# Performance work log

Measured on AMD Instinct MI355X. Metric: run time of the kernel, lower is better.

Reference implementation:

```python
import jax, jax.numpy as jnp
import numpy as np

WS = 4           # window_size
NUM_HEADS = 4
LN_EPS = 1e-5


def setup_inputs() -> dict:
    key = jax.random.key(0)
    ks = jax.random.split(key, 8)
    d = 256
    s = 0.02
    return {
        "feature": jax.random.normal(ks[0], (8, d, 127, 127), dtype=jnp.float32),
        "ln_w": jnp.ones((d,), jnp.float32),
        "ln_b": jnp.zeros((d,), jnp.float32),
        "in_w": jax.random.normal(ks[1], (3 * d, d), jnp.float32) * s,
        "in_b": jnp.zeros((3 * d,), jnp.float32),
        "out_w": jax.random.normal(ks[2], (d, d), jnp.float32) * s,
        "out_b": jnp.zeros((d,), jnp.float32),
        "proj_w": jax.random.normal(ks[3], (d, d), jnp.float32) * s,
        "proj_b": jnp.zeros((d,), jnp.float32),
    }


def reference(feature, ln_w, ln_b, in_w, in_b, out_w, out_b, proj_w, proj_b):
    B, C, H, W = feature.shape
    ws = WS
    pad_h = (-H) % ws
    pad_w = (-W) % ws
    x = jnp.pad(feature, ((0, 0), (0, 0), (0, pad_h), (0, pad_w)))
    Hp, Wp = H + pad_h, W + pad_w
    nh, nw = Hp // ws, Wp // ws
    # NCHW -> NHWC -> windows [B*nh*nw, ws*ws, C]
    x = x.transpose(0, 2, 3, 1)
    win = (x.reshape(B, nh, ws, nw, ws, C)
            .transpose(0, 1, 3, 2, 4, 5)
            .reshape(-1, ws * ws, C))
    # LayerNorm (ddof=0, matches torch)
    mu = win.mean(-1, keepdims=True)
    var = win.var(-1, keepdims=True)
    xn = (win - mu) / jnp.sqrt(var + LN_EPS) * ln_w + ln_b
    # fused QKV projection, then split heads
    qkv = xn @ in_w.T + in_b
    q, k, v = jnp.split(qkv, 3, axis=-1)
    hd = C // NUM_HEADS
    def heads(t):
        return t.reshape(t.shape[0], t.shape[1], NUM_HEADS, hd).transpose(0, 2, 1, 3)
    q, k, v = heads(q), heads(k), heads(v)
    scores = jnp.einsum('bhqd,bhkd->bhqk', q, k) / np.float32(np.sqrt(hd))
    a = jax.nn.softmax(scores, axis=-1)
    o = jnp.einsum('bhqk,bhkd->bhqd', a, v)
    o = o.transpose(0, 2, 1, 3).reshape(-1, ws * ws, C)
    o = o @ out_w.T + out_b
    # residual + Linear + exact GELU
    y = win + jax.nn.gelu(o @ proj_w.T + proj_b, approximate=False)
    # windows -> NHWC, crop padding, -> NCHW
    y = (y.reshape(B, nh, nw, ws, ws, C)
          .transpose(0, 1, 3, 2, 4, 5)
          .reshape(B, Hp, Wp, C))
    return y[:, :H, :W, :].transpose(0, 3, 1, 2)
```

## Files before the change

kernel.cpp:

```cpp
#include <hip/hip_runtime.h>

typedef _Float16 f16;
typedef __attribute__((ext_vector_type(4))) _Float16 half4;
typedef __attribute__((ext_vector_type(8))) _Float16 half8;
typedef __attribute__((ext_vector_type(4))) float f32x4;
typedef unsigned short u16;

#define MFMA32(a,b,c) __builtin_amdgcn_mfma_f32_16x16x32_f16(a,b,c,0,0,0)
#define MFMA16(a,b,c) __builtin_amdgcn_mfma_f32_16x16x16f16(a,b,c,0,0,0)

#define W_IN0   0
#define W_OUT0  196608
#define W_PROJ0 262144
#define X0      327680
#define QK0     33882112ull
#define VT0     100990976ull

__device__ __forceinline__ float gelu_f(float x) {
    float z = x * 0.70710678118f;
    float az = fabsf(z);
    float t = 1.f / (1.f + 0.3275911f * az);
    float e = __expf(-z * z);
    float poly = ((((1.061405429f * t - 1.453152027f) * t + 1.421413741f) * t
                   - 0.284496736f) * t + 0.254829592f) * t;
    float er = 1.f - poly * e;
    er = copysignf(er, z);
    return 0.5f * x * (1.f + er);
}

__global__ void k0_cast(const float* __restrict__ iw, const float* __restrict__ ow,
                        const float* __restrict__ pw, f16* __restrict__ W) {
    int i = blockIdx.x * 256 + threadIdx.x;
    if (i < 196608) W[W_IN0 + i] = (f16)iw[i];
    if (i < 16384) {
        const int s = i & 8191;
        const float* src = (i < 8192) ? ow : pw;
        f16* dst = W + ((i < 8192) ? W_OUT0 : W_PROJ0);
        const int r = s >> 5, sp = s & 31;
        const int kc = (sp >> 2) ^ (r & 7);
        const int gg = sp & 3;
        const int c0 = kc * 32 + gg * 4;
        f32x4 v0 = *(const f32x4*)(src + r * 256 + c0);
        f32x4 v1 = *(const f32x4*)(src + r * 256 + c0 + 16);
        half8 o;
#pragma unroll
        for (int j = 0; j < 4; ++j) { o[j] = (f16)v0[j]; o[j + 4] = (f16)v1[j]; }
        *(half8*)(dst + (r >> 5) * 8192 + (r & 31) * 256 + sp * 8) = o;
    }
}

__global__ __launch_bounds__(256, 4)
void k1_pack(const float* __restrict__ feat, const float* __restrict__ lnw,
             const float* __restrict__ lnb, f16* __restrict__ X) {
    const int tid = threadIdx.x, lane = tid & 63, hh = tid >> 6;
    const int bid = blockIdx.x;
    const int jh = bid & 3, wi = (bid >> 2) & 31, bb = bid >> 7;
    const int h0 = wi * 4, w0 = jh * 32;
    const int wl4 = lane & 7, cg = lane >> 3;
    const int h = h0 + hh, wb = w0 + wl4 * 4;
    const bool hok = (h < 127);
    const bool edge = (wb + 3) >= 127;
    const size_t bbase = (size_t)bb * (256 * 127 * 127);
    const int c0 = cg * 32;
    const float* p0 = feat + bbase + (size_t)c0 * 16129 + (size_t)h * 127 + wb;

    half4 arr[32];
    float ss[4] = {0.f, 0.f, 0.f, 0.f}, qq[4] = {0.f, 0.f, 0.f, 0.f};
    if (hok && !edge) {
#pragma unroll
        for (int i = 0; i < 32; ++i) {
            f32x4 v = *(const f32x4*)(p0 + (size_t)i * 16129);
            half4 hv;
#pragma unroll
            for (int e = 0; e < 4; ++e) { ss[e] += v[e]; qq[e] += v[e] * v[e]; hv[e] = (f16)v[e]; }
            arr[i] = hv;
        }
    } else if (hok) {
#pragma unroll
        for (int i = 0; i < 32; ++i) {
            const float* pi = p0 + (size_t)i * 16129;
            half4 hv;
#pragma unroll
            for (int e = 0; e < 3; ++e) { float v = pi[e]; ss[e] += v; qq[e] += v * v; hv[e] = (f16)v; }
            hv[3] = (f16)0.f;
            arr[i] = hv;
        }
    } else {
#pragma unroll
        for (int i = 0; i < 32; ++i) {
            half4 hv; hv[0] = hv[1] = hv[2] = hv[3] = (f16)0.f; arr[i] = hv;
        }
    }
#pragma unroll
    for (int e = 0; e < 4; ++e) {
        ss[e] += __shfl_xor(ss[e], 8);  qq[e] += __shfl_xor(qq[e], 8);
        ss[e] += __shfl_xor(ss[e], 16); qq[e] += __shfl_xor(qq[e], 16);
        ss[e] += __shfl_xor(ss[e], 32); qq[e] += __shfl_xor(qq[e], 32);
    }
    float mu[4], rs[4];
#pragma unroll
    for (int e = 0; e < 4; ++e) {
        mu[e] = ss[e] * (1.f / 256.f);
        rs[e] = rsqrtf(qq[e] * (1.f / 256.f) - mu[e] * mu[e] + 1e-5f);
    }
#pragma unroll
    for (int q = 0; q < 4; ++q) {
        f32x4 lw0 = *(const f32x4*)(lnw + c0 + q * 8);
        f32x4 lw1 = *(const f32x4*)(lnw + c0 + q * 8 + 4);
        f32x4 lb0 = *(const f32x4*)(lnb + c0 + q * 8);
        f32x4 lb1 = *(const f32x4*)(lnb + c0 + q * 8 + 4);
#pragma unroll
        for (int e = 0; e < 4; ++e) {
            const int m = wl4 * 16 + hh * 4 + e;
            f16* xrow = X + ((size_t)bid * 128 + m) * 256 + c0;
            half8 o;
#pragma unroll
            for (int j = 0; j < 4; ++j) {
                o[j]     = (f16)(((float)arr[q * 8 + j][e]     - mu[e]) * rs[e] * lw0[j] + lb0[j]);
                o[j + 4] = (f16)(((float)arr[q * 8 + j + 4][e] - mu[e]) * rs[e] * lw1[j] + lb1[j]);
            }
            *(half8*)(xrow + q * 8) = o;
        }
    }
}

__global__ __launch_bounds__(512, 2)
void k2_qkv(const f16* __restrict__ X, const f16* __restrict__ win,
            const float* __restrict__ inb, f16* __restrict__ QK, f16* __restrict__ VT) {
    __shared__ __align__(16) char sm[49152];
    const int tid = threadIdx.x, lane = tid & 63, wv = tid >> 6;
    const int nwg = gridDim.x;
    const int bid = (blockIdx.x & 7) * (nwg >> 3) + (blockIdx.x >> 3);
    const int mt = bid / 6, nb = bid % 6;
    const size_t Mbase = (size_t)mt * 256;
    const int n0 = nb * 128;
    const int wm = wv >> 1, wn = wv & 1;
    const int c = lane & 15, g = lane >> 4;
    const int chs = (lane & 3) ^ ((lane >> 3) & 3);

    f32x4 acc[4][4];
#pragma unroll
    for (int a = 0; a < 4; ++a)
#pragma unroll
        for (int b = 0; b < 4; ++b) acc[a][b] = f32x4{0.f, 0.f, 0.f, 0.f};

    auto stage = [&](int step, int bsel) {
        const f16* As = X + Mbase * 256 + step * 32;
        const f16* Bs = win + (size_t)n0 * 256 + step * 32;
        char* base = sm + bsel * 24576;
#pragma unroll
        for (int p = 0; p < 2; ++p) {
            int row = p * 128 + wv * 16 + (lane >> 2);
            __builtin_amdgcn_global_load_lds(
                (const __attribute__((address_space(1))) unsigned int*)(As + (size_t)row * 256 + chs * 8),
                (__attribute__((address_space(3))) unsigned int*)(base + p * 8192 + wv * 1024),
                16, 0, 0);
        }
        {
            int row = wv * 16 + (lane >> 2);
            __builtin_amdgcn_global_load_lds(
                (const __attribute__((address_space(1))) unsigned int*)(Bs + (size_t)row * 256 + chs * 8),
                (__attribute__((address_space(3))) unsigned int*)(base + 16384 + wv * 1024),
                16, 0, 0);
        }
    };
    const int rsl = (g ^ ((c >> 1) & 3)) * 16;
    auto compute = [&](int bsel) {
        char* base = sm + bsel * 24576;
        half8 a[4], b[4];
#pragma unroll
        for (int mi = 0; mi < 4; ++mi) {
            int row = wm * 64 + mi * 16 + c;
            a[mi] = *(half8*)(base + row * 64 + rsl);
        }
#pragma unroll
        for (int nt = 0; nt < 4; ++nt) {
            int row = wn * 64 + nt * 16 + c;
            b[nt] = *(half8*)(base + 16384 + row * 64 + rsl);
        }
#pragma unroll
        for (int mi = 0; mi < 4; ++mi)
#pragma unroll
            for (int nt = 0; nt < 4; ++nt)
                acc[mi][nt] = MFMA32(a[mi], b[nt], acc[mi][nt]);
    };

    stage(0, 0);
    __syncthreads();
#pragma unroll
    for (int s = 0; s < 8; ++s) {
        const int bsel = s & 1;
        if (s < 7) stage(s + 1, bsel ^ 1);
        compute(bsel);
        __syncthreads();
    }

    const f32x4 z4 = {0.f, 0.f, 0.f, 0.f};
    half4 idf;
#pragma unroll
    for (int j = 0; j < 4; ++j) idf[j] = (f16)((g * 4 + j == c) ? 1.f : 0.f);

    if (n0 < 512) {
#pragma unroll
        for (int mi = 0; mi < 4; ++mi)
#pragma unroll
            for (int nt = 0; nt < 4; ++nt) {
                int n = n0 + wn * 64 + nt * 16 + c;
                float bias = inb[n];
                half4 h;
#pragma unroll
                for (int r = 0; r < 4; ++r) h[r] = (f16)(acc[mi][nt][r] + bias);
                f32x4 t = MFMA16(h, idf, z4);
                half4 o;
#pragma unroll
                for (int r = 0; r < 4; ++r) o[r] = (f16)t[r];
                size_t tok = Mbase + wm * 64 + mi * 16 + c;
                *(half4*)(QK + tok * 512 + (n0 + wn * 64 + nt * 16 + g * 4)) = o;
            }
    } else {
#pragma unroll
        for (int mi = 0; mi < 4; ++mi)
#pragma unroll
            for (int nt = 0; nt < 4; ++nt) {
                int n = n0 + wn * 64 + nt * 16 + c;
                float bias = inb[n];
                half4 h;
#pragma unroll
                for (int r = 0; r < 4; ++r) h[r] = (f16)(acc[mi][nt][r] + bias);
                int d = n - 512;
                size_t tokb = Mbase + wm * 64 + mi * 16;
                size_t winI = tokb >> 4;
                *(half4*)(VT + winI * 4096 + (size_t)d * 16 + g * 4) = h;
            }
    }
}

__global__ __launch_bounds__(512, 2)
void k3_attn(const f16* __restrict__ QK, const f16* __restrict__ VT,
             const f16* __restrict__ wout, const f16* __restrict__ wproj,
             const float* __restrict__ outb, const float* __restrict__ projb,
             f16* __restrict__ G) {
    __shared__ __align__(16) char sm[32768];
    const int tid = threadIdx.x, lane = tid & 63, wv = tid >> 6;
    const int c = lane & 15, g = lane >> 4;
    const size_t win = (size_t)blockIdx.x * 8 + wv;
    const f16* qrow = QK + (win * 16 + c) * 512;
    const f32x4 z4 = {0.f, 0.f, 0.f, 0.f};

    auto stageW = [&](const f16* img, int rc, int bsel) {
#pragma unroll
        for (int q2 = 0; q2 < 2; ++q2) {
            int ia = wv * 2 + q2;
            __builtin_amdgcn_global_load_lds(
                (const __attribute__((address_space(1))) unsigned int*)(img + rc * 8192 + ia * 512 + lane * 8),
                (__attribute__((address_space(3))) unsigned int*)(sm + bsel * 16384 + ia * 1024),
                16, 0, 0);
        }
    };

    stageW(wout, 0, 0);

    half8 ofp[4][2];
#pragma unroll
    for (int hq = 0; hq < 4; ++hq) {
        half8 af0 = *(const half8*)(qrow + 256 + hq * 64 + g * 8);
        half8 af1 = *(const half8*)(qrow + 256 + hq * 64 + 32 + g * 8);
        half8 bq0 = *(const half8*)(qrow + hq * 64 + g * 8);
        half8 bq1 = *(const half8*)(qrow + hq * 64 + 32 + g * 8);
        f32x4 sacc = MFMA32(af0, bq0, z4);
        sacc = MFMA32(af1, bq1, sacc);
        float s0 = sacc[0] * 0.125f, s1 = sacc[1] * 0.125f;
        float s2 = sacc[2] * 0.125f, s3 = sacc[3] * 0.125f;
        float mx = fmaxf(fmaxf(s0, s1), fmaxf(s2, s3));
        mx = fmaxf(mx, __shfl_xor(mx, 16));
        mx = fmaxf(mx, __shfl_xor(mx, 32));
        float p0 = __expf(s0 - mx), p1 = __expf(s1 - mx);
        float p2 = __expf(s2 - mx), p3 = __expf(s3 - mx);
        float sum = p0 + p1 + p2 + p3;
        sum += __shfl_xor(sum, 16);
        sum += __shfl_xor(sum, 32);
        float inv = 1.f / sum;
        half4 pf;
        pf[0] = (f16)(p0 * inv); pf[1] = (f16)(p1 * inv);
        pf[2] = (f16)(p2 * inv); pf[3] = (f16)(p3 * inv);
#pragma unroll
        for (int nt = 0; nt < 4; ++nt) {
            half4 vf = *(const half4*)(VT + win * 4096 + (size_t)(hq * 64 + nt * 16 + c) * 16 + g * 4);
            f32x4 o = MFMA16(vf, pf, z4);
#pragma unroll
            for (int r = 0; r < 4; ++r) ofp[hq][nt >> 1][(nt & 1) * 4 + r] = (f16)o[r];
        }
    }

    const int r0 = c, r1 = 16 + c;
    const int csw = c & 7;
    half8 obp[8];
    __syncthreads();

#pragma unroll
    for (int ch = 0; ch < 8; ++ch) {
        if (ch < 7) stageW(wout, ch + 1, (ch + 1) & 1);
        else        stageW(wproj, 0, (ch + 1) & 1);
        char* base = sm + (ch & 1) * 16384;
        f32x4 a0 = z4, a1 = z4;
#pragma unroll
        for (int kc = 0; kc < 8; ++kc) {
            half8 w0 = *(half8*)(base + r0 * 512 + ((kc ^ csw) * 64 + g * 16));
            a0 = MFMA32(w0, ofp[kc >> 1][kc & 1], a0);
            half8 w1 = *(half8*)(base + r1 * 512 + ((kc ^ csw) * 64 + g * 16));
            a1 = MFMA32(w1, ofp[kc >> 1][kc & 1], a1);
        }
        f32x4 b0 = *(const f32x4*)(outb + ch * 32 + g * 4);
        f32x4 b1 = *(const f32x4*)(outb + ch * 32 + 16 + g * 4);
#pragma unroll
        for (int r = 0; r < 4; ++r) {
            obp[ch][r]     = (f16)(a0[r] + b0[r]);
            obp[ch][4 + r] = (f16)(a1[r] + b1[r]);
        }
        __syncthreads();
    }

#pragma unroll
    for (int pc = 0; pc < 8; ++pc) {
        if (pc < 7) stageW(wproj, pc + 1, (pc + 1) & 1);
        char* base = sm + (pc & 1) * 16384;
        f32x4 a0 = z4, a1 = z4;
#pragma unroll
        for (int kc = 0; kc < 8; ++kc) {
            half8 w0 = *(half8*)(base + r0 * 512 + ((kc ^ csw) * 64 + g * 16));
            a0 = MFMA32(w0, obp[kc], a0);
            half8 w1 = *(half8*)(base + r1 * 512 + ((kc ^ csw) * 64 + g * 16));
            a1 = MFMA32(w1, obp[kc], a1);
        }
        f32x4 b0 = *(const f32x4*)(projb + pc * 32 + g * 4);
        f32x4 b1 = *(const f32x4*)(projb + pc * 32 + 16 + g * 4);
        half4 h0, h1;
#pragma unroll
        for (int r = 0; r < 4; ++r) {
            h0[r] = (f16)gelu_f(a0[r] + b0[r]);
            h1[r] = (f16)gelu_f(a1[r] + b1[r]);
        }
        f16* grow = G + (win * 16 + c) * 256 + pc * 32;
        *(half4*)(grow + g * 4) = h0;
        *(half4*)(grow + 16 + g * 4) = h1;
        if (pc < 7) __syncthreads();
    }
}

__global__ __launch_bounds__(256, 8)
void k4_out(const f16* __restrict__ G, const float* __restrict__ feat, float* __restrict__ outp) {
    const int tid = threadIdx.x;
    const int bid = blockIdx.x;
    const int bb = bid / 127, h = bid % 127;
    const int w = tid & 127;
    const int cq = tid >> 7;
    const bool wok = (w < 127);
    const size_t bbase = (size_t)bb * (256 * 127 * 127);
    const int wi = h >> 2, hh = h & 3;
    const int jh = w >> 5, wl4 = (w >> 2) & 7, e = w & 3;
    const size_t t = ((size_t)((bb * 32 + wi) * 4 + jh)) * 128 + wl4 * 16 + hh * 4 + e;
    const f16* gp = G + t * 256;
    const float* fp = feat + bbase + (size_t)h * 127 + w;
    float* op = outp + bbase + (size_t)h * 127 + w;
#pragma unroll 4
    for (int ci = 0; ci < 32; ++ci) {
        const int ch = ci * 8 + cq * 4;
        if (wok) {
            half4 g4 = *(const half4*)(gp + ch);
#pragma unroll
            for (int j = 0; j < 4; ++j) {
                size_t off = (size_t)(ch + j) * 16129;
                op[off] = fp[off] + (float)g4[j];
            }
        }
    }
}

extern "C" void kernel_launch(void* const* d_in, const int* in_sizes, int n_in,
                              void* d_out, int out_size, void* d_ws, size_t ws_size,
                              hipStream_t stream) {
    const float* feat   = (const float*)d_in[0];
    const float* ln_w   = (const float*)d_in[1];
    const float* ln_b   = (const float*)d_in[2];
    const float* in_w   = (const float*)d_in[3];
    const float* in_b   = (const float*)d_in[4];
    const float* out_w  = (const float*)d_in[5];
    const float* out_b  = (const float*)d_in[6];
    const float* proj_w = (const float*)d_in[7];
    const float* proj_b = (const float*)d_in[8];

    f16* W  = (f16*)d_ws;
    f16* Xb  = W + X0;
    f16* QKb = W + QK0;
    f16* VTb = W + VT0;
    f16* Gb  = Xb;

    k0_cast<<<768, 256, 0, stream>>>(in_w, out_w, proj_w, W);
    k1_pack<<<1024, 256, 0, stream>>>(feat, ln_w, ln_b, Xb);
    k2_qkv<<<3072, 512, 0, stream>>>(Xb, W + W_IN0, in_b, QKb, VTb);
    k3_attn<<<1024, 512, 0, stream>>>(QKb, VTb, W + W_OUT0, W + W_PROJ0, out_b, proj_b, Gb);
    k4_out<<<1016, 256, 0, stream>>>(Gb, feat, (float*)d_out);
}
```

Measured before the change: 380.5 us.

## Read attention output/proj weights directly from global instead of LDS staging

Measured after the change: 482.6 us. +26.8%, slower.

```diff
diff --git a/kernel.cpp b/kernel.cpp
--- a/kernel.cpp
+++ b/kernel.cpp
@@ -235,30 +235,16 @@
     }
 }
 
-__global__ __launch_bounds__(512, 2)
+__global__ __launch_bounds__(256, 3)
 void k3_attn(const f16* __restrict__ QK, const f16* __restrict__ VT,
              const f16* __restrict__ wout, const f16* __restrict__ wproj,
              const float* __restrict__ outb, const float* __restrict__ projb,
              f16* __restrict__ G) {
-    __shared__ __align__(16) char sm[32768];
     const int tid = threadIdx.x, lane = tid & 63, wv = tid >> 6;
     const int c = lane & 15, g = lane >> 4;
-    const size_t win = (size_t)blockIdx.x * 8 + wv;
+    const size_t win = (size_t)blockIdx.x * 4 + wv;
     const f16* qrow = QK + (win * 16 + c) * 512;
     const f32x4 z4 = {0.f, 0.f, 0.f, 0.f};
-
-    auto stageW = [&](const f16* img, int rc, int bsel) {
-#pragma unroll
-        for (int q2 = 0; q2 < 2; ++q2) {
-            int ia = wv * 2 + q2;
-            __builtin_amdgcn_global_load_lds(
-                (const __attribute__((address_space(1))) unsigned int*)(img + rc * 8192 + ia * 512 + lane * 8),
-                (__attribute__((address_space(3))) unsigned int*)(sm + bsel * 16384 + ia * 1024),
-                16, 0, 0);
-        }
-    };
-
-    stageW(wout, 0, 0);
 
     half8 ofp[4][2];
 #pragma unroll
@@ -292,22 +278,21 @@
         }
     }
 
-    const int r0 = c, r1 = 16 + c;
     const int csw = c & 7;
+    const int spo = g * 8;
     half8 obp[8];
-    __syncthreads();
 
 #pragma unroll
     for (int ch = 0; ch < 8; ++ch) {
-        if (ch < 7) stageW(wout, ch + 1, (ch + 1) & 1);
-        else        stageW(wproj, 0, (ch + 1) & 1);
-        char* base = sm + (ch & 1) * 16384;
+        const f16* wb0 = wout + ch * 8192 + c * 256;
+        const f16* wb1 = wb0 + 16 * 256;
         f32x4 a0 = z4, a1 = z4;
 #pragma unroll
         for (int kc = 0; kc < 8; ++kc) {
-            half8 w0 = *(half8*)(base + r0 * 512 + ((kc ^ csw) * 64 + g * 16));
+            int sp = (kc ^ csw) * 32 + spo;
+            half8 w0 = *(const half8*)(wb0 + sp);
             a0 = MFMA32(w0, ofp[kc >> 1][kc & 1], a0);
-            half8 w1 = *(half8*)(base + r1 * 512 + ((kc ^ csw) * 64 + g * 16));
+            half8 w1 = *(const half8*)(wb1 + sp);
             a1 = MFMA32(w1, ofp[kc >> 1][kc & 1], a1);
         }
         f32x4 b0 = *(const f32x4*)(outb + ch * 32 + g * 4);
@@ -317,19 +302,19 @@
             obp[ch][r]     = (f16)(a0[r] + b0[r]);
             obp[ch][4 + r] = (f16)(a1[r] + b1[r]);
         }
-        __syncthreads();
     }
 
 #pragma unroll
     for (int pc = 0; pc < 8; ++pc) {
-        if (pc < 7) stageW(wproj, pc + 1, (pc + 1) & 1);
-        char* base = sm + (pc & 1) * 16384;
+        const f16* wb0 = wproj + pc * 8192 + c * 256;
+        const f16* wb1 = wb0 + 16 * 256;
         f32x4 a0 = z4, a1 = z4;
 #pragma unroll
         for (int kc = 0; kc < 8; ++kc) {
-            half8 w0 = *(half8*)(base + r0 * 512 + ((kc ^ csw) * 64 + g * 16));
+            int sp = (kc ^ csw) * 32 + spo;
+            half8 w0 = *(const half8*)(wb0 + sp);
             a0 = MFMA32(w0, obp[kc], a0);
-            half8 w1 = *(half8*)(base + r1 * 512 + ((kc ^ csw) * 64 + g * 16));
+            half8 w1 = *(const half8*)(wb1 + sp);
             a1 = MFMA32(w1, obp[kc], a1);
         }
         f32x4 b0 = *(const f32x4*)(projb + pc * 32 + g * 4);
@@ -343,7 +328,6 @@
         f16* grow = G + (win * 16 + c) * 256 + pc * 32;
         *(half4*)(grow + g * 4) = h0;
         *(half4*)(grow + 16 + g * 4) = h1;
-        if (pc < 7) __syncthreads();
     }
 }
 
@@ -398,6 +382,6 @@
     k0_cast<<<768, 256, 0, stream>>>(in_w, out_w, proj_w, W);
     k1_pack<<<1024, 256, 0, stream>>>(feat, ln_w, ln_b, Xb);
     k2_qkv<<<3072, 512, 0, stream>>>(Xb, W + W_IN0, in_b, QKb, VTb);
-    k3_attn<<<1024, 512, 0, stream>>>(QKb, VTb, W + W_OUT0, W + W_PROJ0, out_b, proj_b, Gb);
+    k3_attn<<<2048, 256, 0, stream>>>(QKb, VTb, W + W_OUT0, W + W_PROJ0, out_b, proj_b, Gb);
     k4_out<<<1016, 256, 0, stream>>>(Gb, feat, (float*)d_out);
 }
```
